# Kernel tuning notes

Measured on AMD Instinct MI355X. Metric: run time of the kernel, lower is better.

## Reference

```python
import jax, jax.numpy as jnp
import numpy as np

# Config / sizes
N = 20000       # nodes
E = 320000      # edges (avg degree 16)
IN_DIM = 6      # node feature dim
PE = 8          # laplacian PE dims
ED = 4          # edge feature dim
H = 128         # hidden dim
OUT = 4         # output dim
L = 3           # message-passing layers
T = 3           # node types (typed encoders/decoders)


def mlp(z, W1, b1, W2, b2):
    # _make_mlp: Linear -> ReLU -> Linear
    return jax.nn.relu(z @ W1 + b1) @ W2 + b2


def typed_mlp(z, W1, b1, W2, b2, types):
    # W1: [T, Din, H]; compute all T branches, select per-node by type
    h = jax.nn.relu(jnp.einsum('ni,tih->tnh', z, W1) + b1[:, None, :])
    o = jnp.einsum('tnh,tho->tno', h, W2) + b2[:, None, :]
    onehot = jax.nn.one_hot(types, W1.shape[0], dtype=o.dtype)  # [N, T]
    return jnp.einsum('tno,nt->no', o, onehot)


def setup_inputs() -> dict:
    key = jax.random.key(0)
    ks = jax.random.split(key, 40)

    def w(k, shape, fan_in):
        return jax.random.normal(k, shape, dtype=jnp.float32) / np.float32(np.sqrt(fan_in))

    inp = {}
    inp['x'] = jax.random.normal(ks[0], (N, IN_DIM), dtype=jnp.float32)
    inp['pe'] = jax.random.normal(ks[1], (N, PE), dtype=jnp.float32)
    inp['edge_attr'] = jax.random.normal(ks[2], (E, ED), dtype=jnp.float32)
    # typed node encoders: (in_dim+pe_dims) -> H -> H
    inp['enc_W1'] = w(ks[3], (T, IN_DIM + PE, H), IN_DIM + PE)
    inp['enc_b1'] = jnp.zeros((T, H), jnp.float32)
    inp['enc_W2'] = w(ks[4], (T, H, H), H)
    inp['enc_b2'] = jnp.zeros((T, H), jnp.float32)
    # edge encoder: ED -> H -> H
    inp['ee_W1'] = w(ks[5], (ED, H), ED)
    inp['ee_b1'] = jnp.zeros((H,), jnp.float32)
    inp['ee_W2'] = w(ks[6], (H, H), H)
    inp['ee_b2'] = jnp.zeros((H,), jnp.float32)
    # per-layer edge update (3H->H->H), node update (2H->H->H), fusion (H->H->H)
    inp['eu_W1'] = w(ks[7], (L, 3 * H, H), 3 * H)
    inp['eu_b1'] = jnp.zeros((L, H), jnp.float32)
    inp['eu_W2'] = w(ks[8], (L, H, H), H)
    inp['eu_b2'] = jnp.zeros((L, H), jnp.float32)
    inp['nu_W1'] = w(ks[9], (L, 2 * H, H), 2 * H)
    inp['nu_b1'] = jnp.zeros((L, H), jnp.float32)
    inp['nu_W2'] = w(ks[10], (L, H, H), H)
    inp['nu_b2'] = jnp.zeros((L, H), jnp.float32)
    inp['fu_W1'] = w(ks[11], (L, H, H), H)
    inp['fu_b1'] = jnp.zeros((L, H), jnp.float32)
    inp['fu_W2'] = w(ks[12], (L, H, H), H)
    inp['fu_b2'] = jnp.zeros((L, H), jnp.float32)
    # typed decoders: H -> H -> OUT
    inp['dec_W1'] = w(ks[13], (T, H, H), H)
    inp['dec_b1'] = jnp.zeros((T, H), jnp.float32)
    inp['dec_W2'] = w(ks[14], (T, H, OUT), H)
    inp['dec_b2'] = jnp.zeros((T, OUT), jnp.float32)
    # int inputs
    inp['edge_index'] = jax.random.randint(ks[15], (2, E), 0, N)
    inp['node_types'] = jax.random.randint(ks[16], (N,), 0, T)
    return inp


def reference(x, pe, edge_attr,
              enc_W1, enc_b1, enc_W2, enc_b2,
              ee_W1, ee_b1, ee_W2, ee_b2,
              eu_W1, eu_b1, eu_W2, eu_b2,
              nu_W1, nu_b1, nu_W2, nu_b2,
              fu_W1, fu_b1, fu_W2, fu_b2,
              dec_W1, dec_b1, dec_W2, dec_b2,
              edge_index, node_types):
    n = x.shape[0]
    src, dst = edge_index[0], edge_index[1]
    # typed node encode on [x || pe]
    h_nodes = typed_mlp(jnp.concatenate([x, pe], axis=-1),
                        enc_W1, enc_b1, enc_W2, enc_b2, node_types)
    # edge encode
    h_edges = mlp(edge_attr, ee_W1, ee_b1, ee_W2, ee_b2)
    num_layers = eu_W1.shape[0]
    for l in range(num_layers):
        # gather endpoint states, edge MLP, residual on edges
        m_edge = mlp(jnp.concatenate([h_nodes[src], h_nodes[dst], h_edges], axis=-1),
                     eu_W1[l], eu_b1[l], eu_W2[l], eu_b2[l])
        h_edges = h_edges + m_edge
        # scatter-add aggregation to destination nodes (index_add_)
        m_node = jax.ops.segment_sum(h_edges, dst, num_segments=n)
        # node update + residual, then fusion (dropout is eval/identity)
        upd = mlp(jnp.concatenate([h_nodes, m_node], axis=-1),
                  nu_W1[l], nu_b1[l], nu_W2[l], nu_b2[l])
        local = h_nodes + upd
        h_nodes = mlp(local, fu_W1[l], fu_b1[l], fu_W2[l], fu_b2[l])
    # typed decode
    out = typed_mlp(h_nodes, dec_W1, dec_b1, dec_W2, dec_b2, node_types)
    return out
```

## Files before the change

kernel.cpp:

```cpp
#include <hip/hip_runtime.h>
#include <hip/hip_bf16.h>

typedef __hip_bfloat16 bf16;
typedef __attribute__((ext_vector_type(8))) short short8;
typedef __attribute__((ext_vector_type(4))) float floatx4;

#define HDIM 128
#define NCANON 27

__device__ __forceinline__ float b2f(bf16 v) { return __bfloat162float(v); }
__device__ __forceinline__ float s2f(short s) {
  return __uint_as_float(((unsigned int)(unsigned short)s) << 16);
}
__device__ __forceinline__ short f2s(float f) {
  return (short)__bfloat16_as_ushort(__float2bfloat16(f));
}

struct CanonDesc {
  const void* src[NCANON];
  int prefix[NCANON + 1];
};

__global__ void canon_kernel(CanonDesc d, const unsigned short* __restrict__ xraw,
                             int* __restrict__ flagOut, bf16* __restrict__ out, int total,
                             int canonBlocks, uint4* __restrict__ zbase, int zquads) {
  int tid = threadIdx.x;
  if (blockIdx.x >= canonBlocks) {
    int i = (blockIdx.x - canonBlocks) * 256 + tid;
    if (i < zquads) { uint4 z = {0u, 0u, 0u, 0u}; zbase[i] = z; }
    return;
  }
  __shared__ int sflag;
  if (tid < 64) {
    unsigned short u = xraw[2 * tid];
    int e = (u >> 7) & 0xFF;
    int ok = (u == 0) || (e >= 100 && e <= 140);
    unsigned long long m = __ballot(ok);
    if (tid == 0) sflag = (__popcll(m) >= 48) ? 1 : 0;
  }
  __syncthreads();
  int isBf = sflag;
  if (blockIdx.x == 0 && tid == 0) flagOut[0] = isBf;
  int t = blockIdx.x * 256 + tid;
  if (t >= total) return;
  int lo = 0, hi = NCANON;
  while (lo + 1 < hi) { int mid = (lo + hi) >> 1; if (d.prefix[mid] <= t) lo = mid; else hi = mid; }
  int off = t - d.prefix[lo];
  out[t] = isBf ? ((const bf16*)d.src[lo])[off]
                : __float2bfloat16(((const float*)d.src[lo])[off]);
}

__global__ void __launch_bounds__(1024) hist_tsort_kernel(
    const int* __restrict__ dst, int* __restrict__ cnt, int E, int hb,
    const int* __restrict__ types, int* __restrict__ ts, int* __restrict__ perm, int n) {
  if (blockIdx.x < hb) {
    int e = blockIdx.x * 1024 + threadIdx.x;
    if (e < E) atomicAdd(&cnt[dst[e]], 1);
    return;
  }
  __shared__ int wc[16][3];
  __shared__ int base[3];
  int tid = threadIdx.x, lane = tid & 63, wave = tid >> 6;
  int c0 = 0, c1 = 0, c2 = 0;
  for (int i = tid; i < n; i += 1024) {
    int t = types[i];
    c0 += (t == 0); c1 += (t == 1); c2 += (t == 2);
  }
  #pragma unroll
  for (int d = 32; d; d >>= 1) {
    c0 += __shfl_down(c0, d); c1 += __shfl_down(c1, d); c2 += __shfl_down(c2, d);
  }
  if (lane == 0) { wc[wave][0] = c0; wc[wave][1] = c1; wc[wave][2] = c2; }
  __syncthreads();
  if (tid == 0) {
    int t0 = 0, t1 = 0;
    for (int w = 0; w < 16; w++) { t0 += wc[w][0]; t1 += wc[w][1]; }
    ts[0] = 0; ts[1] = t0; ts[2] = t0 + t1; ts[3] = n;
    base[0] = 0; base[1] = t0; base[2] = t0 + t1;
  }
  __syncthreads();
  for (int i0 = 0; i0 < n; i0 += 1024) {
    int i = i0 + tid;
    int t = (i < n) ? types[i] : -1;
    unsigned long long m0 = __ballot(t == 0);
    unsigned long long m1 = __ballot(t == 1);
    unsigned long long m2 = __ballot(t == 2);
    if (lane == 0) { wc[wave][0] = __popcll(m0); wc[wave][1] = __popcll(m1); wc[wave][2] = __popcll(m2); }
    __syncthreads();
    if (i < n) {
      unsigned long long mt = (t == 0) ? m0 : ((t == 1) ? m1 : m2);
      unsigned long long below = (lane == 0) ? 0ull : ((1ull << lane) - 1ull);
      int r = __popcll(mt & below);
      int woff = 0;
      for (int w = 0; w < wave; w++) woff += wc[w][t];
      perm[base[t] + woff + r] = i;
    }
    __syncthreads();
    if (tid == 0) {
      int a0 = 0, a1 = 0, a2 = 0;
      for (int w = 0; w < 16; w++) { a0 += wc[w][0]; a1 += wc[w][1]; a2 += wc[w][2]; }
      base[0] += a0; base[1] += a1; base[2] += a2;
    }
    __syncthreads();
  }
}

__global__ void scan1_kernel(const int* __restrict__ cnt, int* __restrict__ bsum, int n) {
  int tid = threadIdx.x, lane = tid & 63, wave = tid >> 6;
  int i = blockIdx.x * 256 + tid;
  int v = (i < n) ? cnt[i] : 0;
  #pragma unroll
  for (int d = 32; d; d >>= 1) v += __shfl_down(v, d);
  __shared__ int ws[4];
  if (lane == 0) ws[wave] = v;
  __syncthreads();
  if (tid == 0) bsum[blockIdx.x] = ws[0] + ws[1] + ws[2] + ws[3];
}

__global__ void scan2_kernel(int* __restrict__ bsum, int nb) {
  int lane = threadIdx.x;
  int a0 = (lane < nb) ? bsum[lane] : 0;
  int b0 = (64 + lane < nb) ? bsum[64 + lane] : 0;
  int a = a0, b = b0;
  #pragma unroll
  for (int d = 1; d < 64; d <<= 1) { int t = __shfl_up(a, d); if (lane >= d) a += t; }
  int totA = __shfl(a, 63);
  #pragma unroll
  for (int d = 1; d < 64; d <<= 1) { int t = __shfl_up(b, d); if (lane >= d) b += t; }
  int totB = __shfl(b, 63);
  if (lane < nb) bsum[lane] = a - a0;
  if (64 + lane < nb) bsum[64 + lane] = b - b0 + totA;
  if (lane == 0) bsum[nb] = totA + totB;
}

__global__ void scan3_kernel(const int* __restrict__ cnt, const int* __restrict__ bsum,
                             int* __restrict__ row_start, int n, int nb) {
  __shared__ int sh[256];
  int tid = threadIdx.x;
  int i = blockIdx.x * 256 + tid;
  int v = (i < n) ? cnt[i] : 0;
  sh[tid] = v;
  __syncthreads();
  #pragma unroll
  for (int off = 1; off < 256; off <<= 1) {
    int t = (tid >= off) ? sh[tid - off] : 0;
    __syncthreads();
    sh[tid] += t;
    __syncthreads();
  }
  if (i < n) row_start[i] = bsum[blockIdx.x] + sh[tid] - v;
  if (blockIdx.x == 0 && tid == 0) row_start[n] = bsum[nb];
}

__global__ void scatter_kernel(const int* __restrict__ src, const int* __restrict__ dst,
                               const int* __restrict__ row_start, int* __restrict__ cursor,
                               const bf16* __restrict__ ea, bf16* __restrict__ eaS,
                               int* __restrict__ srcS, int* __restrict__ dstS, int E) {
  int e = blockIdx.x * 256 + threadIdx.x;
  if (e < E) {
    int d = dst[e];
    int pos = row_start[d] + atomicAdd(&cursor[d], 1);
    srcS[pos] = src[e];
    dstS[pos] = d;
    *(uint2*)(eaS + (size_t)pos * 4) = *(const uint2*)(ea + (size_t)e * 4);
  }
}

struct PackJob { const bf16* src; bf16* dst; int Ksrc; int KS; int srcCols; };
struct PackJobs { PackJob j[40]; };

__global__ void pack_all_kernel(PackJobs J) {
  PackJob job = J.j[blockIdx.y];
  int idx = blockIdx.x * 256 + threadIdx.x;
  int total = 8 * job.KS * 64;
  if (idx >= total) return;
  int lane = idx & 63;
  int ks = (idx >> 6) % job.KS;
  int ct = idx / (64 * job.KS);
  bf16* o = job.dst + (size_t)idx * 8;
  int ncol = ct * 16 + (lane & 15);
  int kb = ks * 32 + ((lane >> 4) & 3) * 8;
  #pragma unroll
  for (int jj = 0; jj < 8; jj++) {
    int k = kb + jj;
    o[jj] = (k < job.Ksrc && ncol < job.srcCols)
              ? job.src[(size_t)k * job.srcCols + ncol] : __float2bfloat16(0.f);
  }
}

__global__ void __launch_bounds__(256) ygemm_kernel(
    const bf16* __restrict__ X,
    const bf16* __restrict__ WpA, const bf16* __restrict__ WpB,
    bf16* __restrict__ outA, bf16* __restrict__ outB,
    float* __restrict__ mnode, int M) {
  const bf16* Wp = blockIdx.y ? WpB : WpA;
  bf16* outp = blockIdx.y ? outB : outA;
  constexpr int BM = 64, RT = 4, SK = 136;
  __shared__ bf16 Zt[BM * SK];
  const int tid = threadIdx.x;
  const int lane = tid & 63, wave = tid >> 6, colq = lane & 15, quad = lane >> 4;
  const int row0 = blockIdx.x * BM;
  if (blockIdx.y == 0) {
    float4 z = {0.f, 0.f, 0.f, 0.f};
    for (int i = tid; i < BM * 32; i += 256) {
      int row = i >> 5, q = i & 31;
      int gr = row0 + row;
      if (gr < M) *(float4*)(mnode + (size_t)gr * HDIM + q * 4) = z;
    }
  }
  {
    int row = tid >> 2, sub = tid & 3;
    int gr = row0 + row;
    bool ok = gr < M;
    #pragma unroll
    for (int j = 0; j < 4; j++) {
      int seg = j * 4 + sub;
      uint4 v = {0u, 0u, 0u, 0u};
      if (ok) v = *(const uint4*)(X + (size_t)gr * HDIM + seg * 8);
      *(uint4*)(&Zt[row * SK + seg * 8]) = v;
    }
  }
  __syncthreads();
  floatx4 acc[RT][2];
  #pragma unroll
  for (int rt = 0; rt < RT; rt++)
    #pragma unroll
    for (int c = 0; c < 2; c++) acc[rt][c] = (floatx4){0.f, 0.f, 0.f, 0.f};
  #pragma unroll
  for (int ks = 0; ks < 4; ks++) {
    short8 bfr0 = *(const short8*)(Wp + (((size_t)(wave * 2 + 0) * 4 + ks) * 64 + lane) * 8);
    short8 bfr1 = *(const short8*)(Wp + (((size_t)(wave * 2 + 1) * 4 + ks) * 64 + lane) * 8);
    #pragma unroll
    for (int rt = 0; rt < RT; rt++) {
      short8 a = *(const short8*)(&Zt[(rt * 16 + colq) * SK + ks * 32 + quad * 8]);
      acc[rt][0] = __builtin_amdgcn_mfma_f32_16x16x32_bf16(a, bfr0, acc[rt][0], 0, 0, 0);
      acc[rt][1] = __builtin_amdgcn_mfma_f32_16x16x32_bf16(a, bfr1, acc[rt][1], 0, 0, 0);
    }
  }
  #pragma unroll
  for (int c = 0; c < 2; c++) {
    int col = wave * 32 + c * 16 + colq;
    #pragma unroll
    for (int rt = 0; rt < RT; rt++)
      #pragma unroll
      for (int r = 0; r < 4; r++) {
        int grow = row0 + rt * 16 + quad * 4 + r;
        if (grow < M) outp[(size_t)grow * HDIM + col] = __float2bfloat16(acc[rt][c][r]);
      }
  }
}

template<int BM, bool WRITE_HE>
__global__ void __launch_bounds__(256) eu_kernel(
    const bf16* __restrict__ he, const bf16* __restrict__ ysrc, const bf16* __restrict__ ydst,
    const int* __restrict__ srcS, const int* __restrict__ dstS,
    const bf16* __restrict__ W1p, const bf16* __restrict__ b1v,
    const bf16* __restrict__ W2p, const bf16* __restrict__ b2v,
    bf16* __restrict__ outp, float* __restrict__ mnode, int M) {
  constexpr int RT = BM / 16;
  constexpr int SK = 264;
  __shared__ bf16 Zt[BM * SK];
  __shared__ int dstLds[BM];
  const int tid = threadIdx.x;
  const int lane = tid & 63, wave = tid >> 6, colq = lane & 15, quad = lane >> 4;
  const int row0 = blockIdx.x * BM;
  constexpr int TPR = 256 / BM;
  {
    int row = tid / TPR, sub = tid % TPR;
    int gr = row0 + row;
    bool ok = gr < M;
    int g0 = ok ? srcS[gr] : 0;
    int g1 = ok ? dstS[gr] : 0;
    if (sub == 0) dstLds[row] = ok ? g1 : -1;
    #pragma unroll
    for (int j = 0; j < 32 / TPR; j++) {
      int c = j * TPR + sub;
      int part = c >> 4, seg = c & 15;
      if (part == 0) {
        short8 o = {0, 0, 0, 0, 0, 0, 0, 0};
        if (ok) {
          short8 a = *(const short8*)(ysrc + (size_t)g0 * HDIM + seg * 8);
          short8 b = *(const short8*)(ydst + (size_t)g1 * HDIM + seg * 8);
          #pragma unroll
          for (int k = 0; k < 8; k++) o[k] = f2s(s2f(a[k]) + s2f(b[k]));
        }
        *(short8*)(&Zt[row * SK + seg * 8]) = o;
      } else {
        uint4 v = {0u, 0u, 0u, 0u};
        if (ok) v = *(const uint4*)(he + (size_t)gr * HDIM + seg * 8);
        *(uint4*)(&Zt[row * SK + 128 + seg * 8]) = v;
      }
    }
  }
  __syncthreads();

  floatx4 acc[RT][2];
  #pragma unroll
  for (int rt = 0; rt < RT; rt++)
    #pragma unroll
    for (int c = 0; c < 2; c++) acc[rt][c] = (floatx4){0.f, 0.f, 0.f, 0.f};
  #pragma unroll
  for (int ks = 0; ks < 4; ks++) {
    short8 bfr0 = *(const short8*)(W1p + (((size_t)(wave * 2 + 0) * 4 + ks) * 64 + lane) * 8);
    short8 bfr1 = *(const short8*)(W1p + (((size_t)(wave * 2 + 1) * 4 + ks) * 64 + lane) * 8);
    #pragma unroll
    for (int rt = 0; rt < RT; rt++) {
      short8 a = *(const short8*)(&Zt[(rt * 16 + colq) * SK + 128 + ks * 32 + quad * 8]);
      acc[rt][0] = __builtin_amdgcn_mfma_f32_16x16x32_bf16(a, bfr0, acc[rt][0], 0, 0, 0);
      acc[rt][1] = __builtin_amdgcn_mfma_f32_16x16x32_bf16(a, bfr1, acc[rt][1], 0, 0, 0);
    }
  }
  #pragma unroll
  for (int c = 0; c < 2; c++) {
    int col = wave * 32 + c * 16 + colq;
    float bv = b2f(b1v[col]);
    #pragma unroll
    for (int rt = 0; rt < RT; rt++)
      #pragma unroll
      for (int r = 0; r < 4; r++) {
        int lrow = rt * 16 + quad * 4 + r;
        float v = acc[rt][c][r] + bv + b2f(Zt[lrow * SK + col]);
        Zt[lrow * SK + col] = __float2bfloat16(fmaxf(v, 0.f));
      }
  }
  __syncthreads();

  floatx4 acc2[RT][2];
  #pragma unroll
  for (int rt = 0; rt < RT; rt++)
    #pragma unroll
    for (int c = 0; c < 2; c++) acc2[rt][c] = (floatx4){0.f, 0.f, 0.f, 0.f};
  #pragma unroll
  for (int ks = 0; ks < 4; ks++) {
    short8 bfr0 = *(const short8*)(W2p + (((size_t)(wave * 2 + 0) * 4 + ks) * 64 + lane) * 8);
    short8 bfr1 = *(const short8*)(W2p + (((size_t)(wave * 2 + 1) * 4 + ks) * 64 + lane) * 8);
    #pragma unroll
    for (int rt = 0; rt < RT; rt++) {
      short8 a = *(const short8*)(&Zt[(rt * 16 + colq) * SK + ks * 32 + quad * 8]);
      acc2[rt][0] = __builtin_amdgcn_mfma_f32_16x16x32_bf16(a, bfr0, acc2[rt][0], 0, 0, 0);
      acc2[rt][1] = __builtin_amdgcn_mfma_f32_16x16x32_bf16(a, bfr1, acc2[rt][1], 0, 0, 0);
    }
  }
  #pragma unroll
  for (int c = 0; c < 2; c++) {
    int col = wave * 32 + c * 16 + colq;
    float bv = b2f(b2v[col]);
    #pragma unroll
    for (int rt = 0; rt < RT; rt++)
      #pragma unroll
      for (int r = 0; r < 4; r++) {
        int lrow = rt * 16 + quad * 4 + r;
        int grow = row0 + lrow;
        float v = acc2[rt][c][r] + bv + b2f(Zt[lrow * SK + 128 + col]);
        bf16 vb = __float2bfloat16(v);
        Zt[lrow * SK + 128 + col] = vb;
        if (WRITE_HE && grow < M) outp[(size_t)grow * HDIM + col] = vb;
      }
  }
  __syncthreads();

  {
    int col = tid & 127;
    int half = tid >> 7;
    int rbeg = half * (BM / 2), rend = rbeg + (BM / 2);
    float s = 0.f;
    int runDst = dstLds[rbeg];
    bool touchStart = true;
    for (int r = rbeg; r < rend; r++) {
      int d = dstLds[r];
      if (d != runDst) {
        if (runDst >= 0) {
          float* mp = &mnode[(size_t)runDst * HDIM + col];
          if (touchStart) atomicAdd(mp, s); else *mp = s;
        }
        runDst = d; s = 0.f; touchStart = false;
      }
      s += b2f(Zt[r * SK + 128 + col]);
    }
    if (runDst >= 0) atomicAdd(&mnode[(size_t)runDst * HDIM + col], s);
  }
}

__global__ void __launch_bounds__(256) node_kernel(
    const bf16* __restrict__ h_nodes, float* __restrict__ mnode,
    const bf16* __restrict__ nuW1, const bf16* __restrict__ nuB1,
    const bf16* __restrict__ nuW2, const bf16* __restrict__ nuB2,
    const bf16* __restrict__ fuW1, const bf16* __restrict__ fuB1,
    const bf16* __restrict__ fuW2, const bf16* __restrict__ fuB2,
    const bf16* __restrict__ yW1a, const bf16* __restrict__ yW1b,
    bf16* __restrict__ ysA, bf16* __restrict__ ysB,
    bf16* __restrict__ outp, int M) {
  constexpr int BM = 64, RT = 4, SK = 264;
  __shared__ bf16 Zt[BM * SK];
  const int tid = threadIdx.x;
  const int lane = tid & 63, wave = tid >> 6, colq = lane & 15, quad = lane >> 4;
  const int row0 = blockIdx.x * BM;
  {
    int row = tid >> 2, sub = tid & 3;
    int gr = row0 + row;
    bool ok = gr < M;
    float4 z4 = {0.f, 0.f, 0.f, 0.f};
    #pragma unroll
    for (int j = 0; j < 8; j++) {
      int c = j * 4 + sub;
      int part = c >> 4, seg = c & 15;
      if (part == 0) {
        uint4 v = {0u, 0u, 0u, 0u};
        if (ok) v = *(const uint4*)(h_nodes + (size_t)gr * HDIM + seg * 8);
        *(uint4*)(&Zt[row * SK + seg * 8]) = v;
      } else {
        short8 o = {0, 0, 0, 0, 0, 0, 0, 0};
        if (ok) {
          float* mp = mnode + (size_t)gr * HDIM + seg * 8;
          #pragma unroll
          for (int k = 0; k < 8; k++) o[k] = f2s(mp[k]);
          if (yW1a) { *(float4*)(mp) = z4; *(float4*)(mp + 4) = z4; }
        }
        *(short8*)(&Zt[row * SK + 128 + seg * 8]) = o;
      }
    }
  }
  __syncthreads();

  floatx4 acc[RT][2];
  #pragma unroll
  for (int rt = 0; rt < RT; rt++)
    #pragma unroll
    for (int c = 0; c < 2; c++) acc[rt][c] = (floatx4){0.f, 0.f, 0.f, 0.f};
  #pragma unroll
  for (int ks = 0; ks < 8; ks++) {
    short8 bfr0 = *(const short8*)(nuW1 + (((size_t)(wave * 2 + 0) * 8 + ks) * 64 + lane) * 8);
    short8 bfr1 = *(const short8*)(nuW1 + (((size_t)(wave * 2 + 1) * 8 + ks) * 64 + lane) * 8);
    #pragma unroll
    for (int rt = 0; rt < RT; rt++) {
      short8 a = *(const short8*)(&Zt[(rt * 16 + colq) * SK + ks * 32 + quad * 8]);
      acc[rt][0] = __builtin_amdgcn_mfma_f32_16x16x32_bf16(a, bfr0, acc[rt][0], 0, 0, 0);
      acc[rt][1] = __builtin_amdgcn_mfma_f32_16x16x32_bf16(a, bfr1, acc[rt][1], 0, 0, 0);
    }
  }
  __syncthreads();
  #pragma unroll
  for (int c = 0; c < 2; c++) {
    int col = wave * 32 + c * 16 + colq;
    float bv = b2f(nuB1[col]);
    #pragma unroll
    for (int rt = 0; rt < RT; rt++)
      #pragma unroll
      for (int r = 0; r < 4; r++)
        Zt[(rt * 16 + quad * 4 + r) * SK + 128 + col] =
            __float2bfloat16(fmaxf(acc[rt][c][r] + bv, 0.f));
  }
  __syncthreads();

  #pragma unroll
  for (int rt = 0; rt < RT; rt++)
    #pragma unroll
    for (int c = 0; c < 2; c++) acc[rt][c] = (floatx4){0.f, 0.f, 0.f, 0.f};
  #pragma unroll
  for (int ks = 0; ks < 4; ks++) {
    short8 bfr0 = *(const short8*)(nuW2 + (((size_t)(wave * 2 + 0) * 4 + ks) * 64 + lane) * 8);
    short8 bfr1 = *(const short8*)(nuW2 + (((size_t)(wave * 2 + 1) * 4 + ks) * 64 + lane) * 8);
    #pragma unroll
    for (int rt = 0; rt < RT; rt++) {
      short8 a = *(const short8*)(&Zt[(rt * 16 + colq) * SK + 128 + ks * 32 + quad * 8]);
      acc[rt][0] = __builtin_amdgcn_mfma_f32_16x16x32_bf16(a, bfr0, acc[rt][0], 0, 0, 0);
      acc[rt][1] = __builtin_amdgcn_mfma_f32_16x16x32_bf16(a, bfr1, acc[rt][1], 0, 0, 0);
    }
  }
  #pragma unroll
  for (int c = 0; c < 2; c++) {
    int col = wave * 32 + c * 16 + colq;
    float bv = b2f(nuB2[col]);
    #pragma unroll
    for (int rt = 0; rt < RT; rt++)
      #pragma unroll
      for (int r = 0; r < 4; r++) {
        int lrow = rt * 16 + quad * 4 + r;
        float v = acc[rt][c][r] + bv + b2f(Zt[lrow * SK + col]);
        Zt[lrow * SK + col] = __float2bfloat16(v);
      }
  }
  __syncthreads();

  #pragma unroll
  for (int rt = 0; rt < RT; rt++)
    #pragma unroll
    for (int c = 0; c < 2; c++) acc[rt][c] = (floatx4){0.f, 0.f, 0.f, 0.f};
  #pragma unroll
  for (int ks = 0; ks < 4; ks++) {
    short8 bfr0 = *(const short8*)(fuW1 + (((size_t)(wave * 2 + 0) * 4 + ks) * 64 + lane) * 8);
    short8 bfr1 = *(const short8*)(fuW1 + (((size_t)(wave * 2 + 1) * 4 + ks) * 64 + lane) * 8);
    #pragma unroll
    for (int rt = 0; rt < RT; rt++) {
      short8 a = *(const short8*)(&Zt[(rt * 16 + colq) * SK + ks * 32 + quad * 8]);
      acc[rt][0] = __builtin_amdgcn_mfma_f32_16x16x32_bf16(a, bfr0, acc[rt][0], 0, 0, 0);
      acc[rt][1] = __builtin_amdgcn_mfma_f32_16x16x32_bf16(a, bfr1, acc[rt][1], 0, 0, 0);
    }
  }
  #pragma unroll
  for (int c = 0; c < 2; c++) {
    int col = wave * 32 + c * 16 + colq;
    float bv = b2f(fuB1[col]);
    #pragma unroll
    for (int rt = 0; rt < RT; rt++)
      #pragma unroll
      for (int r = 0; r < 4; r++)
        Zt[(rt * 16 + quad * 4 + r) * SK + 128 + col] =
            __float2bfloat16(fmaxf(acc[rt][c][r] + bv, 0.f));
  }
  __syncthreads();

  #pragma unroll
  for (int rt = 0; rt < RT; rt++)
    #pragma unroll
    for (int c = 0; c < 2; c++) acc[rt][c] = (floatx4){0.f, 0.f, 0.f, 0.f};
  #pragma unroll
  for (int ks = 0; ks < 4; ks++) {
    short8 bfr0 = *(const short8*)(fuW2 + (((size_t)(wave * 2 + 0) * 4 + ks) * 64 + lane) * 8);
    short8 bfr1 = *(const short8*)(fuW2 + (((size_t)(wave * 2 + 1) * 4 + ks) * 64 + lane) * 8);
    #pragma unroll
    for (int rt = 0; rt < RT; rt++) {
      short8 a = *(const short8*)(&Zt[(rt * 16 + colq) * SK + 128 + ks * 32 + quad * 8]);
      acc[rt][0] = __builtin_amdgcn_mfma_f32_16x16x32_bf16(a, bfr0, acc[rt][0], 0, 0, 0);
      acc[rt][1] = __builtin_amdgcn_mfma_f32_16x16x32_bf16(a, bfr1, acc[rt][1], 0, 0, 0);
    }
  }
  #pragma unroll
  for (int c = 0; c < 2; c++) {
    int col = wave * 32 + c * 16 + colq;
    float bv = b2f(fuB2[col]);
    #pragma unroll
    for (int rt = 0; rt < RT; rt++)
      #pragma unroll
      for (int r = 0; r < 4; r++) {
        int lrow = rt * 16 + quad * 4 + r;
        int grow = row0 + lrow;
        bf16 hb = __float2bfloat16(acc[rt][c][r] + bv);
        Zt[lrow * SK + col] = hb;
        if (grow < M) outp[(size_t)grow * HDIM + col] = hb;
      }
  }
  if (!yW1a) return;
  __syncthreads();

  #pragma unroll
  for (int which = 0; which < 2; which++) {
    const bf16* Wp = which ? yW1b : yW1a;
    bf16* outy = which ? ysB : ysA;
    #pragma unroll
    for (int rt = 0; rt < RT; rt++)
      #pragma unroll
      for (int c = 0; c < 2; c++) acc[rt][c] = (floatx4){0.f, 0.f, 0.f, 0.f};
    #pragma unroll
    for (int ks = 0; ks < 4; ks++) {
      short8 bfr0 = *(const short8*)(Wp + (((size_t)(wave * 2 + 0) * 4 + ks) * 64 + lane) * 8);
      short8 bfr1 = *(const short8*)(Wp + (((size_t)(wave * 2 + 1) * 4 + ks) * 64 + lane) * 8);
      #pragma unroll
      for (int rt = 0; rt < RT; rt++) {
        short8 a = *(const short8*)(&Zt[(rt * 16 + colq) * SK + ks * 32 + quad * 8]);
        acc[rt][0] = __builtin_amdgcn_mfma_f32_16x16x32_bf16(a, bfr0, acc[rt][0], 0, 0, 0);
        acc[rt][1] = __builtin_amdgcn_mfma_f32_16x16x32_bf16(a, bfr1, acc[rt][1], 0, 0, 0);
      }
    }
    #pragma unroll
    for (int c = 0; c < 2; c++) {
      int col = wave * 32 + c * 16 + colq;
      #pragma unroll
      for (int rt = 0; rt < RT; rt++)
        #pragma unroll
        for (int r = 0; r < 4; r++) {
          int grow = row0 + rt * 16 + quad * 4 + r;
          if (grow < M) outy[(size_t)grow * HDIM + col] = __float2bfloat16(acc[rt][c][r]);
        }
    }
  }
}

__global__ void __launch_bounds__(256) encee_kernel(
    int eeBlocks, int ngrid64,
    const bf16* __restrict__ eaS,
    const bf16* __restrict__ eeW1, const bf16* __restrict__ eeB1,
    const bf16* __restrict__ eeW2, const bf16* __restrict__ eeB2,
    bf16* __restrict__ h_edges, int E,
    const bf16* __restrict__ x, const bf16* __restrict__ pe,
    const int* __restrict__ perm, const int* __restrict__ ts,
    const bf16* __restrict__ encW1, const bf16* __restrict__ encB1,
    const bf16* __restrict__ encW2, const bf16* __restrict__ encB2,
    bf16* __restrict__ h_nodes) {
  __shared__ bf16 smem[128 * 136];
  __shared__ int gIdx[64];
  const int tid = threadIdx.x;
  const int lane = tid & 63, wave = tid >> 6, colq = lane & 15, quad = lane >> 4;

  if (blockIdx.x < eeBlocks) {
    constexpr int BM = 128, RT = 8, SK = 136;
    bf16* Zt = smem;
    const int row0 = blockIdx.x * BM;
    for (int i = tid; i < BM * 4; i += 256) {
      int row = i >> 2, seg = i & 3;
      int gr = row0 + row;
      uint4 val = {0u, 0u, 0u, 0u};
      if (seg == 0 && gr < E) {
        uint2 v = *(const uint2*)(eaS + (size_t)gr * 4);
        val.x = v.x; val.y = v.y;
      }
      *(uint4*)(&Zt[row * SK + seg * 8]) = val;
    }
    __syncthreads();
    floatx4 acc[RT][2];
    #pragma unroll
    for (int rt = 0; rt < RT; rt++)
      #pragma unroll
      for (int c = 0; c < 2; c++) acc[rt][c] = (floatx4){0.f, 0.f, 0.f, 0.f};
    {
      short8 bfr0 = *(const short8*)(eeW1 + (((size_t)(wave * 2 + 0)) * 64 + lane) * 8);
      short8 bfr1 = *(const short8*)(eeW1 + (((size_t)(wave * 2 + 1)) * 64 + lane) * 8);
      #pragma unroll
      for (int rt = 0; rt < RT; rt++) {
        short8 a = *(const short8*)(&Zt[(rt * 16 + colq) * SK + quad * 8]);
        acc[rt][0] = __builtin_amdgcn_mfma_f32_16x16x32_bf16(a, bfr0, acc[rt][0], 0, 0, 0);
        acc[rt][1] = __builtin_amdgcn_mfma_f32_16x16x32_bf16(a, bfr1, acc[rt][1], 0, 0, 0);
      }
    }
    __syncthreads();
    #pragma unroll
    for (int c = 0; c < 2; c++) {
      int col = wave * 32 + c * 16 + colq;
      float bv = b2f(eeB1[col]);
      #pragma unroll
      for (int rt = 0; rt < RT; rt++)
        #pragma unroll
        for (int r = 0; r < 4; r++)
          Zt[(rt * 16 + quad * 4 + r) * SK + col] =
              __float2bfloat16(fmaxf(acc[rt][c][r] + bv, 0.f));
    }
    __syncthreads();
    floatx4 acc2[RT][2];
    #pragma unroll
    for (int rt = 0; rt < RT; rt++)
      #pragma unroll
      for (int c = 0; c < 2; c++) acc2[rt][c] = (floatx4){0.f, 0.f, 0.f, 0.f};
    #pragma unroll
    for (int ks = 0; ks < 4; ks++) {
      short8 bfr0 = *(const short8*)(eeW2 + (((size_t)(wave * 2 + 0) * 4 + ks) * 64 + lane) * 8);
      short8 bfr1 = *(const short8*)(eeW2 + (((size_t)(wave * 2 + 1) * 4 + ks) * 64 + lane) * 8);
      #pragma unroll
      for (int rt = 0; rt < RT; rt++) {
        short8 a = *(const short8*)(&Zt[(rt * 16 + colq) * SK + ks * 32 + quad * 8]);
        acc2[rt][0] = __builtin_amdgcn_mfma_f32_16x16x32_bf16(a, bfr0, acc2[rt][0], 0, 0, 0);
        acc2[rt][1] = __builtin_amdgcn_mfma_f32_16x16x32_bf16(a, bfr1, acc2[rt][1], 0, 0, 0);
      }
    }
    #pragma unroll
    for (int c = 0; c < 2; c++) {
      int col = wave * 32 + c * 16 + colq;
      float bv = b2f(eeB2[col]);
      #pragma unroll
      for (int rt = 0; rt < RT; rt++)
        #pragma unroll
        for (int r = 0; r < 4; r++) {
          int grow = row0 + rt * 16 + quad * 4 + r;
          if (grow < E)
            h_edges[(size_t)grow * HDIM + col] = __float2bfloat16(acc2[rt][c][r] + bv);
        }
    }
    return;
  }

  {
    constexpr int BM = 64, RT = 4, SK = 40, HS = 136;
    bf16* Zt = smem;
    bf16* Hid = smem + BM * SK;
    int idx = blockIdx.x - eeBlocks;
    int t = idx / ngrid64;
    int bx = idx - t * ngrid64;
    int rs = ts[t], re = ts[t + 1];
    int row0 = rs + bx * BM;
    if (row0 >= re) return;
    for (int i = tid; i < BM; i += 256) gIdx[i] = (row0 + i < re) ? perm[row0 + i] : -1;
    __syncthreads();
    for (int i = tid; i < BM * 32; i += 256) {
      int row = i >> 5, k = i & 31;
      int g = gIdx[row];
      bf16 v = __float2bfloat16(0.f);
      if (g >= 0 && k < 14) v = (k < 6) ? x[(size_t)g * 6 + k] : pe[(size_t)g * 8 + (k - 6)];
      Zt[row * SK + k] = v;
    }
    __syncthreads();
    const bf16* W1t = encW1 + (size_t)t * 4096;
    const bf16* W2t = encW2 + (size_t)t * 16384;
    floatx4 acc[RT][2];
    #pragma unroll
    for (int rt = 0; rt < RT; rt++)
      #pragma unroll
      for (int c = 0; c < 2; c++) acc[rt][c] = (floatx4){0.f, 0.f, 0.f, 0.f};
    {
      short8 bfr0 = *(const short8*)(W1t + (((size_t)(wave * 2 + 0)) * 64 + lane) * 8);
      short8 bfr1 = *(const short8*)(W1t + (((size_t)(wave * 2 + 1)) * 64 + lane) * 8);
      #pragma unroll
      for (int rt = 0; rt < RT; rt++) {
        short8 a = *(const short8*)(&Zt[(rt * 16 + colq) * SK + quad * 8]);
        acc[rt][0] = __builtin_amdgcn_mfma_f32_16x16x32_bf16(a, bfr0, acc[rt][0], 0, 0, 0);
        acc[rt][1] = __builtin_amdgcn_mfma_f32_16x16x32_bf16(a, bfr1, acc[rt][1], 0, 0, 0);
      }
    }
    #pragma unroll
    for (int c = 0; c < 2; c++) {
      int col = wave * 32 + c * 16 + colq;
      float bv = b2f(encB1[t * HDIM + col]);
      #pragma unroll
      for (int rt = 0; rt < RT; rt++)
        #pragma unroll
        for (int r = 0; r < 4; r++)
          Hid[(rt * 16 + quad * 4 + r) * HS + col] =
              __float2bfloat16(fmaxf(acc[rt][c][r] + bv, 0.f));
    }
    __syncthreads();
    floatx4 acc2[RT][2];
    #pragma unroll
    for (int rt = 0; rt < RT; rt++)
      #pragma unroll
      for (int c = 0; c < 2; c++) acc2[rt][c] = (floatx4){0.f, 0.f, 0.f, 0.f};
    #pragma unroll
    for (int ks = 0; ks < 4; ks++) {
      short8 bfr0 = *(const short8*)(W2t + (((size_t)(wave * 2 + 0) * 4 + ks) * 64 + lane) * 8);
      short8 bfr1 = *(const short8*)(W2t + (((size_t)(wave * 2 + 1) * 4 + ks) * 64 + lane) * 8);
      #pragma unroll
      for (int rt = 0; rt < RT; rt++) {
        short8 a = *(const short8*)(&Hid[(rt * 16 + colq) * HS + ks * 32 + quad * 8]);
        acc2[rt][0] = __builtin_amdgcn_mfma_f32_16x16x32_bf16(a, bfr0, acc2[rt][0], 0, 0, 0);
        acc2[rt][1] = __builtin_amdgcn_mfma_f32_16x16x32_bf16(a, bfr1, acc2[rt][1], 0, 0, 0);
      }
    }
    #pragma unroll
    for (int c = 0; c < 2; c++) {
      int col = wave * 32 + c * 16 + colq;
      float bv = b2f(encB2[t * HDIM + col]);
      #pragma unroll
      for (int rt = 0; rt < RT; rt++)
        #pragma unroll
        for (int r = 0; r < 4; r++) {
          int g = gIdx[rt * 16 + quad * 4 + r];
          if (g >= 0) h_nodes[(size_t)g * HDIM + col] = __float2bfloat16(acc2[rt][c][r] + bv);
        }
    }
  }
}

__global__ void __launch_bounds__(256) dec_kernel(
    const bf16* __restrict__ in0,
    const int* __restrict__ perm, const int* __restrict__ ts, const int* __restrict__ flagp,
    const bf16* __restrict__ W1p, const bf16* __restrict__ b1v,
    const bf16* __restrict__ W2p, const bf16* __restrict__ b2v,
    void* __restrict__ outp) {
  constexpr int BM = 64, RT = 4, SK = 136, HS = 136;
  int t = blockIdx.y;
  int rs = ts[t], re = ts[t + 1];
  int row0 = rs + blockIdx.x * BM;
  if (row0 >= re) return;
  __shared__ bf16 Zt[BM * SK];
  __shared__ bf16 Hid[BM * HS];
  __shared__ int gIdx[BM];
  const int tid = threadIdx.x;
  const int lane = tid & 63, wave = tid >> 6, colq = lane & 15, quad = lane >> 4;
  for (int i = tid; i < BM; i += 256) gIdx[i] = (row0 + i < re) ? perm[row0 + i] : -1;
  __syncthreads();
  {
    int row = tid >> 2, sub = tid & 3;
    int g = gIdx[row];
    #pragma unroll
    for (int j = 0; j < 4; j++) {
      int seg = j * 4 + sub;
      uint4 v = {0u, 0u, 0u, 0u};
      if (g >= 0) v = *(const uint4*)(in0 + (size_t)g * HDIM + seg * 8);
      *(uint4*)(&Zt[row * SK + seg * 8]) = v;
    }
  }
  __syncthreads();
  const bf16* W1t = W1p + (size_t)t * 16384;
  const bf16* W2t = W2p + (size_t)t * 16384;
  floatx4 acc[RT][2];
  #pragma unroll
  for (int rt = 0; rt < RT; rt++)
    #pragma unroll
    for (int c = 0; c < 2; c++) acc[rt][c] = (floatx4){0.f, 0.f, 0.f, 0.f};
  #pragma unroll
  for (int ks = 0; ks < 4; ks++) {
    short8 bfr0 = *(const short8*)(W1t + (((size_t)(wave * 2 + 0) * 4 + ks) * 64 + lane) * 8);
    short8 bfr1 = *(const short8*)(W1t + (((size_t)(wave * 2 + 1) * 4 + ks) * 64 + lane) * 8);
    #pragma unroll
    for (int rt = 0; rt < RT; rt++) {
      short8 a = *(const short8*)(&Zt[(rt * 16 + colq) * SK + ks * 32 + quad * 8]);
      acc[rt][0] = __builtin_amdgcn_mfma_f32_16x16x32_bf16(a, bfr0, acc[rt][0], 0, 0, 0);
      acc[rt][1] = __builtin_amdgcn_mfma_f32_16x16x32_bf16(a, bfr1, acc[rt][1], 0, 0, 0);
    }
  }
  #pragma unroll
  for (int c = 0; c < 2; c++) {
    int col = wave * 32 + c * 16 + colq;
    float bv = b2f(b1v[t * HDIM + col]);
    #pragma unroll
    for (int rt = 0; rt < RT; rt++)
      #pragma unroll
      for (int r = 0; r < 4; r++)
        Hid[(rt * 16 + quad * 4 + r) * HS + col] =
            __float2bfloat16(fmaxf(acc[rt][c][r] + bv, 0.f));
  }
  __syncthreads();
  floatx4 acc2[RT];
  #pragma unroll
  for (int rt = 0; rt < RT; rt++) acc2[rt] = (floatx4){0.f, 0.f, 0.f, 0.f};
  #pragma unroll
  for (int ks = 0; ks < 4; ks++) {
    short8 bfr0 = *(const short8*)(W2t + (((size_t)0 * 4 + ks) * 64 + lane) * 8);
    #pragma unroll
    for (int rt = 0; rt < RT; rt++) {
      short8 a = *(const short8*)(&Hid[(rt * 16 + colq) * HS + ks * 32 + quad * 8]);
      acc2[rt] = __builtin_amdgcn_mfma_f32_16x16x32_bf16(a, bfr0, acc2[rt], 0, 0, 0);
    }
  }
  if (wave == 0 && colq < 4) {
    int isBf = flagp[0];
    float bv = b2f(b2v[t * 4 + colq]);
    #pragma unroll
    for (int rt = 0; rt < RT; rt++)
      #pragma unroll
      for (int r = 0; r < 4; r++) {
        int g = gIdx[rt * 16 + quad * 4 + r];
        if (g >= 0) {
          float v = acc2[rt][r] + bv;
          if (isBf) ((bf16*)outp)[(size_t)g * 4 + colq] = __float2bfloat16(v);
          else      ((float*)outp)[(size_t)g * 4 + colq] = v;
        }
      }
  }
}

extern "C" void kernel_launch(void* const* d_in, const int* in_sizes, int n_in,
                              void* d_out, int out_size, void* d_ws, size_t ws_size,
                              hipStream_t stream) {
  const int* edge_index = (const int*)d_in[27];
  const int* node_types = (const int*)d_in[28];
  const int N = in_sizes[28];
  const int E = in_sizes[2] / 4;
  const int L = in_sizes[12] / HDIM;
  const int* srcI = edge_index;
  const int* dstI = edge_index + E;

  CanonDesc cd;
  int total = 0;
  for (int i = 0; i < NCANON; i++) { cd.src[i] = d_in[i]; cd.prefix[i] = total; total += in_sizes[i]; }
  cd.prefix[NCANON] = total;

  char* wsb = (char*)d_ws;
  size_t off = 0;
  auto alloc = [&](size_t bytes) -> void* {
    void* p = wsb + off;
    off += (bytes + 255) & ~(size_t)255;
    return p;
  };
  int*  flag      = (int*)alloc(256);
  bf16* arena     = (bf16*)alloc((size_t)total * 2);
  bf16* h_nodes   = (bf16*)alloc((size_t)N * HDIM * 2);
  bf16* h_edges   = (bf16*)alloc((size_t)E * HDIM * 2);
  float* m_node   = (float*)alloc((size_t)N * HDIM * 4);
  bf16* ysrcb     = (bf16*)alloc((size_t)N * HDIM * 2);
  bf16* ydstb     = (bf16*)alloc((size_t)N * HDIM * 2);
  bf16* eaS       = (bf16*)alloc((size_t)E * 4 * 2);
  int* counts     = (int*)alloc((size_t)N * 4);
  int* cursor     = (int*)alloc((size_t)N * 4);
  int* row_start  = (int*)alloc((size_t)(N + 1) * 4);
  int* bsum       = (int*)alloc(260 * 4);
  int* srcS       = (int*)alloc((size_t)E * 4);
  int* dstS       = (int*)alloc((size_t)E * 4);
  int* tsArr      = (int*)alloc(64);
  int* permT      = (int*)alloc((size_t)N * 4);
  bf16* eeW1p  = (bf16*)alloc(4096 * 2);
  bf16* eeW2p  = (bf16*)alloc(16384 * 2);
  bf16* encW1p = (bf16*)alloc(3 * 4096 * 2);
  bf16* encW2p = (bf16*)alloc(3 * 16384 * 2);
  bf16* decW1p = (bf16*)alloc(3 * 16384 * 2);
  bf16* decW2p = (bf16*)alloc(3 * 16384 * 2);
  bf16* euW1a  = (bf16*)alloc((size_t)L * 16384 * 2);
  bf16* euW1b  = (bf16*)alloc((size_t)L * 16384 * 2);
  bf16* euW1c  = (bf16*)alloc((size_t)L * 16384 * 2);
  bf16* euW2p  = (bf16*)alloc((size_t)L * 16384 * 2);
  bf16* nuW1p  = (bf16*)alloc((size_t)L * 32768 * 2);
  bf16* nuW2p  = (bf16*)alloc((size_t)L * 16384 * 2);
  bf16* fuW1p  = (bf16*)alloc((size_t)L * 16384 * 2);
  bf16* fuW2p  = (bf16*)alloc((size_t)L * 16384 * 2);

  const bf16* cX     = arena + cd.prefix[0];
  const bf16* cPE    = arena + cd.prefix[1];
  const bf16* cEA    = arena + cd.prefix[2];
  const bf16* cEncW1 = arena + cd.prefix[3];
  const bf16* cEncB1 = arena + cd.prefix[4];
  const bf16* cEncW2 = arena + cd.prefix[5];
  const bf16* cEncB2 = arena + cd.prefix[6];
  const bf16* cEeW1  = arena + cd.prefix[7];
  const bf16* cEeB1  = arena + cd.prefix[8];
  const bf16* cEeW2  = arena + cd.prefix[9];
  const bf16* cEeB2  = arena + cd.prefix[10];
  const bf16* cEuW1  = arena + cd.prefix[11];
  const bf16* cEuB1  = arena + cd.prefix[12];
  const bf16* cEuW2  = arena + cd.prefix[13];
  const bf16* cEuB2  = arena + cd.prefix[14];
  const bf16* cNuW1  = arena + cd.prefix[15];
  const bf16* cNuB1  = arena + cd.prefix[16];
  const bf16* cNuW2  = arena + cd.prefix[17];
  const bf16* cNuB2  = arena + cd.prefix[18];
  const bf16* cFuW1  = arena + cd.prefix[19];
  const bf16* cFuB1  = arena + cd.prefix[20];
  const bf16* cFuW2  = arena + cd.prefix[21];
  const bf16* cFuB2  = arena + cd.prefix[22];
  const bf16* cDecW1 = arena + cd.prefix[23];
  const bf16* cDecB1 = arena + cd.prefix[24];
  const bf16* cDecW2 = arena + cd.prefix[25];
  const bf16* cDecB2 = arena + cd.prefix[26];

  int canonBlocks = (total + 255) / 256;
  size_t zbytes = (size_t)((char*)cursor - (char*)counts) + (size_t)N * 4;
  int zquads = (int)(zbytes / 16);
  int zBlocks = (zquads + 255) / 256;
  canon_kernel<<<canonBlocks + zBlocks, 256, 0, stream>>>(
      cd, (const unsigned short*)d_in[0], flag, arena, total, canonBlocks,
      (uint4*)counts, zquads);

  int hb = (E + 1023) / 1024;
  hist_tsort_kernel<<<hb + 1, 1024, 0, stream>>>(dstI, counts, E, hb,
                                                 node_types, tsArr, permT, N);

  PackJobs PJ;
  int nj = 0;
  PJ.j[nj++] = {cEeW1, eeW1p, 4, 1, 128};
  PJ.j[nj++] = {cEeW2, eeW2p, 128, 4, 128};
  for (int l = 0; l < L; l++) {
    const bf16* w1 = cEuW1 + (size_t)l * 384 * HDIM;
    PJ.j[nj++] = {w1,                 euW1a + (size_t)l * 16384, 128, 4, 128};
    PJ.j[nj++] = {w1 + 128 * HDIM,    euW1b + (size_t)l * 16384, 128, 4, 128};
    PJ.j[nj++] = {w1 + 256 * HDIM,    euW1c + (size_t)l * 16384, 128, 4, 128};
    PJ.j[nj++] = {cEuW2 + (size_t)l * HDIM * HDIM, euW2p + (size_t)l * 16384, 128, 4, 128};
    PJ.j[nj++] = {cNuW1 + (size_t)l * 256 * HDIM,  nuW1p + (size_t)l * 32768, 256, 8, 128};
    PJ.j[nj++] = {cNuW2 + (size_t)l * HDIM * HDIM, nuW2p + (size_t)l * 16384, 128, 4, 128};
    PJ.j[nj++] = {cFuW1 + (size_t)l * HDIM * HDIM, fuW1p + (size_t)l * 16384, 128, 4, 128};
    PJ.j[nj++] = {cFuW2 + (size_t)l * HDIM * HDIM, fuW2p + (size_t)l * 16384, 128, 4, 128};
  }
  for (int t = 0; t < 3; t++) {
    PJ.j[nj++] = {cEncW1 + (size_t)t * 14 * HDIM,   encW1p + (size_t)t * 4096, 14, 1, 128};
    PJ.j[nj++] = {cEncW2 + (size_t)t * HDIM * HDIM, encW2p + (size_t)t * 16384, 128, 4, 128};
    PJ.j[nj++] = {cDecW1 + (size_t)t * HDIM * HDIM, decW1p + (size_t)t * 16384, 128, 4, 128};
    PJ.j[nj++] = {cDecW2 + (size_t)t * HDIM * 4,    decW2p + (size_t)t * 16384, 128, 4, 4};
  }
  pack_all_kernel<<<dim3(16, nj), 256, 0, stream>>>(PJ);

  int nb = (N + 255) / 256;
  scan1_kernel<<<nb, 256, 0, stream>>>(counts, bsum, N);
  scan2_kernel<<<1, 64, 0, stream>>>(bsum, nb);
  scan3_kernel<<<nb, 256, 0, stream>>>(counts, bsum, row_start, N, nb);
  scatter_kernel<<<(E + 255) / 256, 256, 0, stream>>>(srcI, dstI, row_start, cursor,
                                                      cEA, eaS, srcS, dstS, E);

  int ngrid64  = (N + 63) / 64;
  int egrid32  = (E + 31) / 32;
  int egrid128 = (E + 127) / 128;

  encee_kernel<<<egrid128 + 3 * ngrid64, 256, 0, stream>>>(
      egrid128, ngrid64,
      eaS, eeW1p, cEeB1, eeW2p, cEeB2, h_edges, E,
      cX, cPE, permT, tsArr, encW1p, cEncB1, encW2p, cEncB2, h_nodes);

  for (int l = 0; l < L; l++) {
    if (l == 0) {
      ygemm_kernel<<<dim3(ngrid64, 2), 256, 0, stream>>>(
          h_nodes, euW1a, euW1b, ysrcb, ydstb, m_node, N);
    }
    if (l + 1 < L) {
      eu_kernel<32, true><<<egrid32, 256, 0, stream>>>(
          h_edges, ysrcb, ydstb, srcS, dstS,
          euW1c + (size_t)l * 16384, cEuB1 + l * HDIM,
          euW2p + (size_t)l * 16384, cEuB2 + l * HDIM, h_edges, m_node, E);
    } else {
      eu_kernel<32, false><<<egrid32, 256, 0, stream>>>(
          h_edges, ysrcb, ydstb, srcS, dstS,
          euW1c + (size_t)l * 16384, cEuB1 + l * HDIM,
          euW2p + (size_t)l * 16384, cEuB2 + l * HDIM, h_edges, m_node, E);
    }
    bool hasNext = (l + 1 < L);
    node_kernel<<<ngrid64, 256, 0, stream>>>(
        h_nodes, m_node,
        nuW1p + (size_t)l * 32768, cNuB1 + l * HDIM,
        nuW2p + (size_t)l * 16384, cNuB2 + l * HDIM,
        fuW1p + (size_t)l * 16384, cFuB1 + l * HDIM,
        fuW2p + (size_t)l * 16384, cFuB2 + l * HDIM,
        hasNext ? euW1a + (size_t)(l + 1) * 16384 : nullptr,
        hasNext ? euW1b + (size_t)(l + 1) * 16384 : nullptr,
        ysrcb, ydstb, h_nodes, N);
  }

  dec_kernel<<<dim3(ngrid64, 3), 256, 0, stream>>>(
      h_nodes, permT, tsArr, flag, decW1p, cDecB1, decW2p, cDecB2, d_out);
  (void)n_in; (void)ws_size;
}
```

Measured before the change: 470.4 us.

## Stage GEMM outputs through LDS for coalesced stores; widen eu_kernel to 512 threads with XCD-aware remap

Several kernels (ygemm, node, encoder-edge, eu) now write MFMA results into shared memory first, then copy full rows to global memory with 16-byte vector stores instead of scattered 2-byte stores. The edge-update kernel moves from 32-row/256-thread blocks to 64-row/512-thread blocks, with each wave owning one 16-column slice. It also remaps block IDs so that contiguous edge tiles land on the same XCD, which should improve L2 locality for the sorted destination rows. The costs are extra __syncthreads barriers and higher LDS use per block, which may reduce occupancy.

Result: no change. 462.2 us (-1.7%).

```diff
diff --git a/kernel.cpp b/kernel.cpp
--- a/kernel.cpp
+++ b/kernel.cpp
@@ -237,44 +237,52 @@
       acc[rt][1] = __builtin_amdgcn_mfma_f32_16x16x32_bf16(a, bfr1, acc[rt][1], 0, 0, 0);
     }
   }
+  __syncthreads();
   #pragma unroll
   for (int c = 0; c < 2; c++) {
     int col = wave * 32 + c * 16 + colq;
     #pragma unroll
     for (int rt = 0; rt < RT; rt++)
       #pragma unroll
-      for (int r = 0; r < 4; r++) {
-        int grow = row0 + rt * 16 + quad * 4 + r;
-        if (grow < M) outp[(size_t)grow * HDIM + col] = __float2bfloat16(acc[rt][c][r]);
-      }
-  }
-}
-
-template<int BM, bool WRITE_HE>
-__global__ void __launch_bounds__(256) eu_kernel(
+      for (int r = 0; r < 4; r++)
+        Zt[(rt * 16 + quad * 4 + r) * SK + col] = __float2bfloat16(acc[rt][c][r]);
+  }
+  __syncthreads();
+  for (int i = tid; i < BM * 16; i += 256) {
+    int row = i >> 4, seg = i & 15;
+    int gr = row0 + row;
+    if (gr < M)
+      *(uint4*)(outp + (size_t)gr * HDIM + seg * 8) = *(const uint4*)(&Zt[row * SK + seg * 8]);
+  }
+}
+
+template<bool WRITE_HE>
+__global__ void __launch_bounds__(512) eu_kernel(
     const bf16* __restrict__ he, const bf16* __restrict__ ysrc, const bf16* __restrict__ ydst,
     const int* __restrict__ srcS, const int* __restrict__ dstS,
     const bf16* __restrict__ W1p, const bf16* __restrict__ b1v,
     const bf16* __restrict__ W2p, const bf16* __restrict__ b2v,
     bf16* __restrict__ outp, float* __restrict__ mnode, int M) {
-  constexpr int RT = BM / 16;
-  constexpr int SK = 264;
+  constexpr int BM = 64, RT = 4, SK = 264;
   __shared__ bf16 Zt[BM * SK];
   __shared__ int dstLds[BM];
   const int tid = threadIdx.x;
   const int lane = tid & 63, wave = tid >> 6, colq = lane & 15, quad = lane >> 4;
-  const int row0 = blockIdx.x * BM;
-  constexpr int TPR = 256 / BM;
+  const int nwg = gridDim.x, bid = blockIdx.x;
+  const int qq = nwg >> 3, rr = nwg & 7;
+  const int xcd = bid & 7, bidx = bid >> 3;
+  const int blk = (xcd < rr ? xcd * (qq + 1) : rr * (qq + 1) + (xcd - rr) * qq) + bidx;
+  const int row0 = blk * BM;
   {
-    int row = tid / TPR, sub = tid % TPR;
+    int row = tid >> 3, sub = tid & 7;
     int gr = row0 + row;
     bool ok = gr < M;
     int g0 = ok ? srcS[gr] : 0;
     int g1 = ok ? dstS[gr] : 0;
     if (sub == 0) dstLds[row] = ok ? g1 : -1;
     #pragma unroll
-    for (int j = 0; j < 32 / TPR; j++) {
-      int c = j * TPR + sub;
+    for (int j = 0; j < 4; j++) {
+      int c = j * 8 + sub;
       int part = c >> 4, seg = c & 15;
       if (part == 0) {
         short8 o = {0, 0, 0, 0, 0, 0, 0, 0};
@@ -294,75 +302,70 @@
   }
   __syncthreads();
 
-  floatx4 acc[RT][2];
-  #pragma unroll
-  for (int rt = 0; rt < RT; rt++)
-    #pragma unroll
-    for (int c = 0; c < 2; c++) acc[rt][c] = (floatx4){0.f, 0.f, 0.f, 0.f};
+  floatx4 acc[RT];
+  #pragma unroll
+  for (int rt = 0; rt < RT; rt++) acc[rt] = (floatx4){0.f, 0.f, 0.f, 0.f};
   #pragma unroll
   for (int ks = 0; ks < 4; ks++) {
-    short8 bfr0 = *(const short8*)(W1p + (((size_t)(wave * 2 + 0) * 4 + ks) * 64 + lane) * 8);
-    short8 bfr1 = *(const short8*)(W1p + (((size_t)(wave * 2 + 1) * 4 + ks) * 64 + lane) * 8);
+    short8 bfr = *(const short8*)(W1p + (((size_t)wave * 4 + ks) * 64 + lane) * 8);
     #pragma unroll
     for (int rt = 0; rt < RT; rt++) {
       short8 a = *(const short8*)(&Zt[(rt * 16 + colq) * SK + 128 + ks * 32 + quad * 8]);
-      acc[rt][0] = __builtin_amdgcn_mfma_f32_16x16x32_bf16(a, bfr0, acc[rt][0], 0, 0, 0);
-      acc[rt][1] = __builtin_amdgcn_mfma_f32_16x16x32_bf16(a, bfr1, acc[rt][1], 0, 0, 0);
-    }
-  }
-  #pragma unroll
-  for (int c = 0; c < 2; c++) {
-    int col = wave * 32 + c * 16 + colq;
+      acc[rt] = __builtin_amdgcn_mfma_f32_16x16x32_bf16(a, bfr, acc[rt], 0, 0, 0);
+    }
+  }
+  {
+    int col = wave * 16 + colq;
     float bv = b2f(b1v[col]);
     #pragma unroll
     for (int rt = 0; rt < RT; rt++)
       #pragma unroll
       for (int r = 0; r < 4; r++) {
         int lrow = rt * 16 + quad * 4 + r;
-        float v = acc[rt][c][r] + bv + b2f(Zt[lrow * SK + col]);
+        float v = acc[rt][r] + bv + b2f(Zt[lrow * SK + col]);
         Zt[lrow * SK + col] = __float2bfloat16(fmaxf(v, 0.f));
       }
   }
   __syncthreads();
 
-  floatx4 acc2[RT][2];
-  #pragma unroll
-  for (int rt = 0; rt < RT; rt++)
-    #pragma unroll
-    for (int c = 0; c < 2; c++) acc2[rt][c] = (floatx4){0.f, 0.f, 0.f, 0.f};
+  #pragma unroll
+  for (int rt = 0; rt < RT; rt++) acc[rt] = (floatx4){0.f, 0.f, 0.f, 0.f};
   #pragma unroll
   for (int ks = 0; ks < 4; ks++) {
-    short8 bfr0 = *(const short8*)(W2p + (((size_t)(wave * 2 + 0) * 4 + ks) * 64 + lane) * 8);
-    short8 bfr1 = *(const short8*)(W2p + (((size_t)(wave * 2 + 1) * 4 + ks) * 64 + lane) * 8);
+    short8 bfr = *(const short8*)(W2p + (((size_t)wave * 4 + ks) * 64 + lane) * 8);
     #pragma unroll
     for (int rt = 0; rt < RT; rt++) {
       short8 a = *(const short8*)(&Zt[(rt * 16 + colq) * SK + ks * 32 + quad * 8]);
-      acc2[rt][0] = __builtin_amdgcn_mfma_f32_16x16x32_bf16(a, bfr0, acc2[rt][0], 0, 0, 0);
-      acc2[rt][1] = __builtin_amdgcn_mfma_f32_16x16x32_bf16(a, bfr1, acc2[rt][1], 0, 0, 0);
-    }
-  }
-  #pragma unroll
-  for (int c = 0; c < 2; c++) {
-    int col = wave * 32 + c * 16 + colq;
+      acc[rt] = __builtin_amdgcn_mfma_f32_16x16x32_bf16(a, bfr, acc[rt], 0, 0, 0);
+    }
+  }
+  {
+    int col = wave * 16 + colq;
     float bv = b2f(b2v[col]);
     #pragma unroll
     for (int rt = 0; rt < RT; rt++)
       #pragma unroll
       for (int r = 0; r < 4; r++) {
         int lrow = rt * 16 + quad * 4 + r;
-        int grow = row0 + lrow;
-        float v = acc2[rt][c][r] + bv + b2f(Zt[lrow * SK + 128 + col]);
-        bf16 vb = __float2bfloat16(v);
-        Zt[lrow * SK + 128 + col] = vb;
-        if (WRITE_HE && grow < M) outp[(size_t)grow * HDIM + col] = vb;
-      }
-  }
-  __syncthreads();
-
+        float v = acc[rt][r] + bv + b2f(Zt[lrow * SK + 128 + col]);
+        Zt[lrow * SK + 128 + col] = __float2bfloat16(v);
+      }
+  }
+  __syncthreads();
+
+  if (WRITE_HE) {
+    #pragma unroll
+    for (int i = tid; i < BM * 16; i += 512) {
+      int row = i >> 4, seg = i & 15;
+      int gr = row0 + row;
+      if (gr < M)
+        *(uint4*)(outp + (size_t)gr * HDIM + seg * 8) = *(const uint4*)(&Zt[row * SK + 128 + seg * 8]);
+    }
+  }
   {
     int col = tid & 127;
-    int half = tid >> 7;
-    int rbeg = half * (BM / 2), rend = rbeg + (BM / 2);
+    int q4 = tid >> 7;
+    int rbeg = q4 * 16, rend = rbeg + 16;
     float s = 0.f;
     int runDst = dstLds[rbeg];
     bool touchStart = true;
@@ -534,14 +537,17 @@
       #pragma unroll
       for (int r = 0; r < 4; r++) {
         int lrow = rt * 16 + quad * 4 + r;
-        int grow = row0 + lrow;
-        bf16 hb = __float2bfloat16(acc[rt][c][r] + bv);
-        Zt[lrow * SK + col] = hb;
-        if (grow < M) outp[(size_t)grow * HDIM + col] = hb;
-      }
+        Zt[lrow * SK + col] = __float2bfloat16(acc[rt][c][r] + bv);
+      }
+  }
+  __syncthreads();
+  for (int i = tid; i < BM * 16; i += 256) {
+    int row = i >> 4, seg = i & 15;
+    int gr = row0 + row;
+    if (gr < M)
+      *(uint4*)(outp + (size_t)gr * HDIM + seg * 8) = *(const uint4*)(&Zt[row * SK + seg * 8]);
   }
   if (!yW1a) return;
-  __syncthreads();
 
   #pragma unroll
   for (int which = 0; which < 2; which++) {
@@ -568,11 +574,17 @@
       #pragma unroll
       for (int rt = 0; rt < RT; rt++)
         #pragma unroll
-        for (int r = 0; r < 4; r++) {
-          int grow = row0 + rt * 16 + quad * 4 + r;
-          if (grow < M) outy[(size_t)grow * HDIM + col] = __float2bfloat16(acc[rt][c][r]);
-        }
-    }
+        for (int r = 0; r < 4; r++)
+          Zt[(rt * 16 + quad * 4 + r) * SK + 128 + col] = __float2bfloat16(acc[rt][c][r]);
+    }
+    __syncthreads();
+    for (int i = tid; i < BM * 16; i += 256) {
+      int row = i >> 4, seg = i & 15;
+      int gr = row0 + row;
+      if (gr < M)
+        *(uint4*)(outy + (size_t)gr * HDIM + seg * 8) = *(const uint4*)(&Zt[row * SK + 128 + seg * 8]);
+    }
+    __syncthreads();
   }
 }
 
@@ -651,6 +663,7 @@
         acc2[rt][1] = __builtin_amdgcn_mfma_f32_16x16x32_bf16(a, bfr1, acc2[rt][1], 0, 0, 0);
       }
     }
+    __syncthreads();
     #pragma unroll
     for (int c = 0; c < 2; c++) {
       int col = wave * 32 + c * 16 + colq;
@@ -658,11 +671,15 @@
       #pragma unroll
       for (int rt = 0; rt < RT; rt++)
         #pragma unroll
-        for (int r = 0; r < 4; r++) {
-          int grow = row0 + rt * 16 + quad * 4 + r;
-          if (grow < E)
-            h_edges[(size_t)grow * HDIM + col] = __float2bfloat16(acc2[rt][c][r] + bv);
-        }
+        for (int r = 0; r < 4; r++)
+          Zt[(rt * 16 + quad * 4 + r) * SK + col] = __float2bfloat16(acc2[rt][c][r] + bv);
+    }
+    __syncthreads();
+    for (int i = tid; i < BM * 16; i += 256) {
+      int row = i >> 4, seg = i & 15;
+      int gr = row0 + row;
+      if (gr < E)
+        *(uint4*)(h_edges + (size_t)gr * HDIM + seg * 8) = *(const uint4*)(&Zt[row * SK + seg * 8]);
     }
     return;
   }
@@ -961,7 +978,7 @@
                                                       cEA, eaS, srcS, dstS, E);
 
   int ngrid64  = (N + 63) / 64;
-  int egrid32  = (E + 31) / 32;
+  int egrid64  = (E + 63) / 64;
   int egrid128 = (E + 127) / 128;
 
   encee_kernel<<<egrid128 + 3 * ngrid64, 256, 0, stream>>>(
@@ -975,12 +992,12 @@
           h_nodes, euW1a, euW1b, ysrcb, ydstb, m_node, N);
     }
     if (l + 1 < L) {
-      eu_kernel<32, true><<<egrid32, 256, 0, stream>>>(
+      eu_kernel<true><<<egrid64, 512, 0, stream>>>(
           h_edges, ysrcb, ydstb, srcS, dstS,
           euW1c + (size_t)l * 16384, cEuB1 + l * HDIM,
           euW2p + (size_t)l * 16384, cEuB2 + l * HDIM, h_edges, m_node, E);
     } else {
-      eu_kernel<32, false><<<egrid32, 256, 0, stream>>>(
+      eu_kernel<false><<<egrid64, 512, 0, stream>>>(
           h_edges, ysrcb, ydstb, srcS, dstS,
           euW1c + (size_t)l * 16384, cEuB1 + l * HDIM,
           euW2p + (size_t)l * 16384, cEuB2 + l * HDIM, h_edges, m_node, E);
```
